# Performance work log

Hardware: AMD Instinct MI355X
Metric: run time of the kernel (lower is better)

## Reference

```python
import jax, jax.numpy as jnp
import numpy as np

RESOLUTIONS = [16, 29, 53, 98, 181, 332, 610, 1120]
FEATURE_DIM = 4
FEATURE_STD = 0.01
BATCH = 4
NUM_SAMPLES = 524288


def setup_inputs() -> dict:
    key = jax.random.key(0)
    keys = jax.random.split(key, len(RESOLUTIONS) + 1)
    coords = jax.random.uniform(keys[0], (BATCH, NUM_SAMPLES, 2), dtype=jnp.float32,
                                minval=-1.0, maxval=1.0)
    inp = {"coords": coords, "lod_idx": len(RESOLUTIONS) - 1}
    for i, (res, k) in enumerate(zip(RESOLUTIONS, keys[1:])):
        inp[f"cb{i}"] = jax.random.normal(k, (FEATURE_DIM, res, res), jnp.float32) * FEATURE_STD
    return inp


def _bilerp(cb, coords, align_corners=True):
    """Bilinear grid_sample of cb [F,R,R] at coords [B,N,2] in [-1,1]. Returns [B,N,F]."""
    res = cb.shape[-1]
    if align_corners:
        p = (coords + 1.0) * 0.5 * (res - 1)  # pixel-space coords
    else:
        p = (coords + 1.0) * 0.5 * res - 0.5
    px, py = p[..., 0], p[..., 1]  # x = width idx, y = height idx (grid_sample convention)
    x0f = jnp.floor(px)
    y0f = jnp.floor(py)
    wx = px - x0f  # [B,N]
    wy = py - y0f
    x0 = jnp.clip(x0f.astype(jnp.int32), 0, res - 1)
    x1 = jnp.clip(x0f.astype(jnp.int32) + 1, 0, res - 1)
    y0 = jnp.clip(y0f.astype(jnp.int32), 0, res - 1)
    y1 = jnp.clip(y0f.astype(jnp.int32) + 1, 0, res - 1)
    # Gathers: advanced indexing on last two axes -> [F, B, N]
    f00 = cb[:, y0, x0]
    f01 = cb[:, y0, x1]
    f10 = cb[:, y1, x0]
    f11 = cb[:, y1, x1]
    w00 = ((1.0 - wx) * (1.0 - wy))[None]
    w01 = (wx * (1.0 - wy))[None]
    w10 = ((1.0 - wx) * wy)[None]
    w11 = (wx * wy)[None]
    out = f00 * w00 + f01 * w01 + f10 * w10 + f11 * w11  # [F,B,N]
    return jnp.moveaxis(out, 0, -1)  # [B,N,F]


def reference(coords, lod_idx, cb0, cb1, cb2, cb3, cb4, cb5, cb6, cb7):
    # lod_idx == max lod: all LODs active. multiscale_type='cat'.
    cbs = [cb0, cb1, cb2, cb3, cb4, cb5, cb6, cb7][: lod_idx + 1]
    feats = [_bilerp(cb, coords, align_corners=True) for cb in cbs]
    return jnp.concatenate(feats, axis=-1)  # [B, N, num_lods*feature_dim]
```

## Files before the change

kernel.cpp:

```cpp
#include <hip/hip_runtime.h>
#include <hip/hip_fp16.h>

#define NLEVELS 8
#define NBANDS  64
#define CHUNK   1024

__constant__ int   c_res[NLEVELS]   = {16, 29, 53, 98, 181, 332, 610, 1120};
__constant__ float c_scale[NLEVELS] = {7.5f, 14.0f, 26.0f, 48.5f, 90.0f, 165.5f, 304.5f, 559.5f};
__constant__ int   c_cum[NLEVELS]   = {0, 256, 1097, 3906, 13510, 46271, 156495, 528595};
#define TOTAL_TEXELS 1782995

typedef float        f32x4 __attribute__((ext_vector_type(4)));
typedef unsigned int u32;
typedef u32          u32x4  __attribute__((ext_vector_type(4)));
typedef u32          u32x4a8 __attribute__((ext_vector_type(4), aligned(8)));

struct CbPtrs { const float* cb[NLEVELS]; };

__device__ __forceinline__ float2 up_h2(u32 v) {
    __half2 h = *reinterpret_cast<__half2*>(&v);
    return __half22float2(h);
}
__device__ __forceinline__ u32 pack_h2(float a, float b) {
    __half2 h = __floats2half2_rn(a, b);
    return *reinterpret_cast<u32*>(&h);
}
__device__ __forceinline__ int band_of(float cy) {
    float v = (cy + 1.0f) * 0.5f;
    int k = (int)(v * (float)NBANDS);
    return min(NBANDS - 1, max(0, k));
}

#define PREP_TBLOCKS 1024
#define PREP_HBLOCKS 512
__global__ __launch_bounds__(256) void prep_kernel(CbPtrs p,
                                                   uint2* __restrict__ tcb,
                                                   const float2* __restrict__ coords,
                                                   u32* __restrict__ gcount, int S) {
    if (blockIdx.x < PREP_TBLOCKS) {
        for (int t = blockIdx.x * 256 + threadIdx.x; t < TOTAL_TEXELS; t += PREP_TBLOCKS * 256) {
            int L = 0;
#pragma unroll
            for (int i = 1; i < NLEVELS; ++i) if (t >= c_cum[i]) L = i;
            int i  = t - c_cum[L];
            int rr = c_res[L] * c_res[L];
            const float* cb = p.cb[L];
            uint2 tex;
            tex.x = pack_h2(cb[i],          cb[i + rr]);
            tex.y = pack_h2(cb[i + 2 * rr], cb[i + 3 * rr]);
            tcb[t] = tex;
        }
    } else {
        __shared__ u32 h[NBANDS];
        for (int i = threadIdx.x; i < NBANDS; i += 256) h[i] = 0u;
        __syncthreads();
        int nb = gridDim.x - PREP_TBLOCKS;
        for (int s = (blockIdx.x - PREP_TBLOCKS) * 256 + threadIdx.x; s < S; s += nb * 256)
            atomicAdd(&h[band_of(coords[s].y)], 1u);
        __syncthreads();
        for (int i = threadIdx.x; i < NBANDS; i += 256)
            if (h[i]) atomicAdd(&gcount[i], h[i]);
    }
}

__global__ __launch_bounds__(256) void scatter_kernel(const float2* __restrict__ coords,
                                                      const u32* __restrict__ gcount,
                                                      u32* __restrict__ gcursor2,
                                                      u32x4* __restrict__ recS, int S) {
    __shared__ u32 h[NBANDS];
    __shared__ u32 bandstart[NBANDS];
    __shared__ u32 rank_base[NBANDS];
    int s0 = blockIdx.x * CHUNK;
    for (int i = threadIdx.x; i < NBANDS; i += 256) h[i] = 0u;
    if (threadIdx.x == 0) {
        u32 acc = 0;
#pragma unroll
        for (int i = 0; i < NBANDS; ++i) { bandstart[i] = acc; acc += gcount[i]; }
    }
    __syncthreads();
    u32 myrank[CHUNK / 256];
    int myk[CHUNK / 256];
    float2 myc[CHUNK / 256];
#pragma unroll
    for (int it = 0; it < CHUNK / 256; ++it) {
        int s = s0 + it * 256 + threadIdx.x;
        if (s < S) {
            float2 c = coords[s];
            int k = band_of(c.y);
            myc[it] = c;
            myk[it] = k;
            myrank[it] = atomicAdd(&h[k], 1u);
        }
    }
    __syncthreads();
    for (int i = threadIdx.x; i < NBANDS; i += 256)
        rank_base[i] = bandstart[i] + (h[i] ? atomicAdd(&gcursor2[i], h[i]) : 0u);
    __syncthreads();
#pragma unroll
    for (int it = 0; it < CHUNK / 256; ++it) {
        int s = s0 + it * 256 + threadIdx.x;
        if (s < S) {
            u32 pos = rank_base[myk[it]] + myrank[it];
            u32x4 r;
            r.x = __float_as_uint(myc[it].x);
            r.y = __float_as_uint(myc[it].y);
            r.z = (u32)s;
            r.w = 0u;
            recS[pos] = r;
        }
    }
}

__global__ __launch_bounds__(256) void grid_sorted8(const u32x4* __restrict__ recS,
                                                    const uint2* __restrict__ tcb,
                                                    f32x4* __restrict__ out, int S) {
    int p  = blockIdx.x;
    int nb = gridDim.x;
    int b  = (p & 7) * (nb >> 3) + (p >> 3);
    int t  = b * 256 + threadIdx.x;
    int s  = t >> 3;
    if (s >= S) return;
    int L  = t & 7;

    u32x4 rec = recS[s];
    float cx = __uint_as_float(rec.x);
    float cy = __uint_as_float(rec.y);
    int  idx = (int)rec.z;

    int   res   = c_res[L];
    float scale = c_scale[L];
    const uint2* __restrict__ base = tcb + c_cum[L];

    float px = (cx + 1.0f) * scale;
    float py = (cy + 1.0f) * scale;
    float xf = floorf(px), yf = floorf(py);
    float wx = px - xf,    wy = py - yf;
    int x0 = (int)xf, y0 = (int)yf;
    int xp = min(max(x0, 0), res - 2);  wx += (float)(x0 - xp);
    int yp = min(max(y0, 0), res - 2);  wy += (float)(y0 - yp);
    const uint2* r0 = base + yp * res + xp;
    u32x4a8 t0 = *(const u32x4a8*)r0;
    u32x4a8 t1 = *(const u32x4a8*)(r0 + res);

    float2 a00 = up_h2(t0.x), b00 = up_h2(t0.y);
    float2 a01 = up_h2(t0.z), b01 = up_h2(t0.w);
    float2 a10 = up_h2(t1.x), b10 = up_h2(t1.y);
    float2 a11 = up_h2(t1.z), b11 = up_h2(t1.w);

    float w00 = (1.0f - wx) * (1.0f - wy);
    float w01 = wx * (1.0f - wy);
    float w10 = (1.0f - wx) * wy;
    float w11 = wx * wy;

    f32x4 r;
    r.x = a00.x * w00 + a01.x * w01 + a10.x * w10 + a11.x * w11;
    r.y = a00.y * w00 + a01.y * w01 + a10.y * w10 + a11.y * w11;
    r.z = b00.x * w00 + b01.x * w01 + b10.x * w10 + b11.x * w11;
    r.w = b00.y * w00 + b01.y * w01 + b10.y * w10 + b11.y * w11;

    out[(size_t)idx * 8 + L] = r;
}

__global__ __launch_bounds__(256) void grid_generic(const float2* __restrict__ coords,
                                                    CbPtrs p, float4* __restrict__ out4,
                                                    int S, int levels) {
    int s = blockIdx.x * 256 + threadIdx.x;
    if (s >= S) return;
    float2 c = coords[s];
    for (int L = 0; L < levels; ++L) {
        int   res   = c_res[L];
        float scale = c_scale[L];
        float px = (c.x + 1.0f) * scale;
        float py = (c.y + 1.0f) * scale;
        float x0f = floorf(px), y0f = floorf(py);
        float wx = px - x0f,    wy = py - y0f;
        int rm1 = res - 1;
        int x0 = min(max((int)x0f, 0), rm1);
        int x1 = min(x0 + 1, rm1);
        int y0 = min(max((int)y0f, 0), rm1);
        int y1 = min(y0 + 1, rm1);
        int i00 = y0 * res + x0, i01 = y0 * res + x1, i10 = y1 * res + x0, i11 = y1 * res + x1;
        float w00 = (1.0f - wx) * (1.0f - wy);
        float w01 = wx * (1.0f - wy);
        float w10 = (1.0f - wx) * wy;
        float w11 = wx * wy;
        float4 r;
        const float* cb = p.cb[L];
        int rr = res * res;
        float* pr = &r.x;
#pragma unroll
        for (int f = 0; f < 4; ++f) {
            const float* cf = cb + f * rr;
            pr[f] = cf[i00] * w00 + cf[i01] * w01 + cf[i10] * w10 + cf[i11] * w11;
        }
        out4[(size_t)s * levels + L] = r;
    }
}

extern "C" void kernel_launch(void* const* d_in, const int* in_sizes, int n_in,
                              void* d_out, int out_size, void* d_ws, size_t ws_size,
                              hipStream_t stream) {
    const float2* coords = (const float2*)d_in[0];
    int S = in_sizes[0] / 2;
    int levels = out_size / (S * 4);

    CbPtrs ptrs;
    for (int i = 0; i < NLEVELS; ++i) ptrs.cb[i] = (const float*)d_in[2 + i];

    size_t tcb_bytes = ((size_t)TOTAL_TEXELS * 8 + 255) & ~(size_t)255;
    size_t cnt_bytes = 512;
    size_t rec_bytes = (size_t)S * 16;
    size_t need = tcb_bytes + cnt_bytes + rec_bytes;

    char*  ws       = (char*)d_ws;
    uint2* tcb      = (uint2*)ws;
    u32*   gcount   = (u32*)(ws + tcb_bytes);
    u32*   gcursor2 = gcount + NBANDS;
    u32x4* recS     = (u32x4*)(ws + tcb_bytes + cnt_bytes);

    if (levels != NLEVELS || ws_size < need) {
        int blocks = (S + 255) / 256;
        grid_generic<<<blocks, 256, 0, stream>>>(coords, ptrs, (float4*)d_out, S, levels);
        return;
    }

    hipMemsetAsync(gcount, 0, cnt_bytes, stream);
    prep_kernel<<<PREP_TBLOCKS + PREP_HBLOCKS, 256, 0, stream>>>(ptrs, tcb, coords, gcount, S);
    int nchunk = (S + CHUNK - 1) / CHUNK;
    scatter_kernel<<<nchunk, 256, 0, stream>>>(coords, gcount, gcursor2, recS, S);

    long long total = (long long)S * 8;
    int nb = (int)((total + 255) / 256);
    nb = ((nb + 7) / 8) * 8;
    grid_sorted8<<<nb, 256, 0, stream>>>(recS, tcb, (f32x4*)d_out, S);
}
```

Before: 166.7 us.

## Replace atomic band sort with per-chunk histograms, scan, and stable ballot scatter

Cuts the number of y-bands from 64 to 8. The global atomic band counters are replaced by per-chunk histograms written to memory, then an exclusive prefix sum in a single-block scan kernel. Scatter now uses wavefront ballots to compute ranks deterministically, so the sort becomes stable and preserves coordinate order within each band. This removes the memset and contended global atomics, and the more sequential record order should help output locality. The cost is an extra kernel launch, a serial single-block scan, coarser bands with possibly worse texture locality, and more syncthreads in scatter.

```diff
diff --git a/kernel.cpp b/kernel.cpp
--- a/kernel.cpp
+++ b/kernel.cpp
@@ -2,7 +2,7 @@
 #include <hip/hip_fp16.h>
 
 #define NLEVELS 8
-#define NBANDS  64
+#define NBANDS  8
 #define CHUNK   1024
 
 __constant__ int   c_res[NLEVELS]   = {16, 29, 53, 98, 181, 332, 610, 1120};
@@ -26,17 +26,16 @@
     return *reinterpret_cast<u32*>(&h);
 }
 __device__ __forceinline__ int band_of(float cy) {
-    float v = (cy + 1.0f) * 0.5f;
-    int k = (int)(v * (float)NBANDS);
+    int k = (int)((cy + 1.0f) * (0.5f * NBANDS));
     return min(NBANDS - 1, max(0, k));
 }
 
 #define PREP_TBLOCKS 1024
-#define PREP_HBLOCKS 512
 __global__ __launch_bounds__(256) void prep_kernel(CbPtrs p,
                                                    uint2* __restrict__ tcb,
                                                    const float2* __restrict__ coords,
-                                                   u32* __restrict__ gcount, int S) {
+                                                   u32* __restrict__ counts,
+                                                   int S, int nchunk) {
     if (blockIdx.x < PREP_TBLOCKS) {
         for (int t = blockIdx.x * 256 + threadIdx.x; t < TOTAL_TEXELS; t += PREP_TBLOCKS * 256) {
             int L = 0;
@@ -51,63 +50,93 @@
             tcb[t] = tex;
         }
     } else {
+        int b = blockIdx.x - PREP_TBLOCKS;
+        if (b >= nchunk) return;
         __shared__ u32 h[NBANDS];
-        for (int i = threadIdx.x; i < NBANDS; i += 256) h[i] = 0u;
-        __syncthreads();
-        int nb = gridDim.x - PREP_TBLOCKS;
-        for (int s = (blockIdx.x - PREP_TBLOCKS) * 256 + threadIdx.x; s < S; s += nb * 256)
-            atomicAdd(&h[band_of(coords[s].y)], 1u);
-        __syncthreads();
-        for (int i = threadIdx.x; i < NBANDS; i += 256)
-            if (h[i]) atomicAdd(&gcount[i], h[i]);
+        if (threadIdx.x < NBANDS) h[threadIdx.x] = 0u;
+        __syncthreads();
+        int s0 = b * CHUNK;
+#pragma unroll
+        for (int it = 0; it < CHUNK / 256; ++it) {
+            int s = s0 + it * 256 + threadIdx.x;
+            if (s < S) atomicAdd(&h[band_of(coords[s].y)], 1u);
+        }
+        __syncthreads();
+        if (threadIdx.x < NBANDS)
+            counts[threadIdx.x * nchunk + b] = h[threadIdx.x];
+    }
+}
+
+__global__ __launch_bounds__(256) void scan_kernel(const u32* __restrict__ counts,
+                                                   u32* __restrict__ base, int N) {
+    __shared__ u32 sums[256];
+    int i = threadIdx.x;
+    int per = (N + 255) / 256;
+    u32 acc = 0;
+    for (int j = 0; j < per; ++j) {
+        int idx = i * per + j;
+        if (idx < N) acc += counts[idx];
+    }
+    sums[i] = acc;
+    __syncthreads();
+    for (int off = 1; off < 256; off <<= 1) {
+        u32 x = (i >= off) ? sums[i - off] : 0u;
+        __syncthreads();
+        sums[i] += x;
+        __syncthreads();
+    }
+    acc = (i == 0) ? 0u : sums[i - 1];
+    for (int j = 0; j < per; ++j) {
+        int idx = i * per + j;
+        if (idx < N) { base[idx] = acc; acc += counts[idx]; }
     }
 }
 
 __global__ __launch_bounds__(256) void scatter_kernel(const float2* __restrict__ coords,
-                                                      const u32* __restrict__ gcount,
-                                                      u32* __restrict__ gcursor2,
-                                                      u32x4* __restrict__ recS, int S) {
-    __shared__ u32 h[NBANDS];
-    __shared__ u32 bandstart[NBANDS];
-    __shared__ u32 rank_base[NBANDS];
-    int s0 = blockIdx.x * CHUNK;
-    for (int i = threadIdx.x; i < NBANDS; i += 256) h[i] = 0u;
-    if (threadIdx.x == 0) {
-        u32 acc = 0;
-#pragma unroll
-        for (int i = 0; i < NBANDS; ++i) { bandstart[i] = acc; acc += gcount[i]; }
-    }
+                                                      const u32* __restrict__ base,
+                                                      u32x4* __restrict__ recS,
+                                                      int S, int nchunk) {
+    __shared__ u32 itbase[NBANDS];
+    __shared__ u32 wcnt[4][NBANDS];
+    int b = blockIdx.x;
+    if (threadIdx.x < NBANDS) itbase[threadIdx.x] = base[threadIdx.x * nchunk + b];
     __syncthreads();
-    u32 myrank[CHUNK / 256];
-    int myk[CHUNK / 256];
-    float2 myc[CHUNK / 256];
+    int s0   = b * CHUNK;
+    int w    = threadIdx.x >> 6;
+    int lane = threadIdx.x & 63;
 #pragma unroll
     for (int it = 0; it < CHUNK / 256; ++it) {
         int s = s0 + it * 256 + threadIdx.x;
-        if (s < S) {
-            float2 c = coords[s];
-            int k = band_of(c.y);
-            myc[it] = c;
-            myk[it] = k;
-            myrank[it] = atomicAdd(&h[k], 1u);
-        }
-    }
-    __syncthreads();
-    for (int i = threadIdx.x; i < NBANDS; i += 256)
-        rank_base[i] = bandstart[i] + (h[i] ? atomicAdd(&gcursor2[i], h[i]) : 0u);
-    __syncthreads();
-#pragma unroll
-    for (int it = 0; it < CHUNK / 256; ++it) {
-        int s = s0 + it * 256 + threadIdx.x;
-        if (s < S) {
-            u32 pos = rank_base[myk[it]] + myrank[it];
+        bool valid = s < S;
+        float2 c = valid ? coords[s] : make_float2(0.0f, 0.0f);
+        int k = band_of(c.y);
+        u32 lr = 0;
+#pragma unroll
+        for (int kk = 0; kk < NBANDS; ++kk) {
+            unsigned long long m = __ballot(valid && (k == kk));
+            if (valid && k == kk)
+                lr = (u32)__popcll(m & ((1ULL << lane) - 1ULL));
+            if (lane == 0) wcnt[w][kk] = (u32)__popcll(m);
+        }
+        __syncthreads();
+        if (threadIdx.x < NBANDS) {
+            int kk = threadIdx.x;
+            u32 acc = itbase[kk];
+#pragma unroll
+            for (int ww = 0; ww < 4; ++ww) { u32 t = wcnt[ww][kk]; wcnt[ww][kk] = acc; acc += t; }
+            itbase[kk] = acc;
+        }
+        __syncthreads();
+        if (valid) {
+            u32 pos = wcnt[w][k] + lr;
             u32x4 r;
-            r.x = __float_as_uint(myc[it].x);
-            r.y = __float_as_uint(myc[it].y);
+            r.x = __float_as_uint(c.x);
+            r.y = __float_as_uint(c.y);
             r.z = (u32)s;
             r.w = 0u;
             recS[pos] = r;
         }
+        __syncthreads();
     }
 }
 
@@ -207,16 +236,18 @@
     CbPtrs ptrs;
     for (int i = 0; i < NLEVELS; ++i) ptrs.cb[i] = (const float*)d_in[2 + i];
 
+    int nchunk = (S + CHUNK - 1) / CHUNK;
+
     size_t tcb_bytes = ((size_t)TOTAL_TEXELS * 8 + 255) & ~(size_t)255;
-    size_t cnt_bytes = 512;
+    size_t cnt_bytes = ((size_t)NBANDS * nchunk * 2 * 4 + 255) & ~(size_t)255;
     size_t rec_bytes = (size_t)S * 16;
     size_t need = tcb_bytes + cnt_bytes + rec_bytes;
 
-    char*  ws       = (char*)d_ws;
-    uint2* tcb      = (uint2*)ws;
-    u32*   gcount   = (u32*)(ws + tcb_bytes);
-    u32*   gcursor2 = gcount + NBANDS;
-    u32x4* recS     = (u32x4*)(ws + tcb_bytes + cnt_bytes);
+    char*  ws     = (char*)d_ws;
+    uint2* tcb    = (uint2*)ws;
+    u32*   counts = (u32*)(ws + tcb_bytes);
+    u32*   basep  = counts + (size_t)NBANDS * nchunk;
+    u32x4* recS   = (u32x4*)(ws + tcb_bytes + cnt_bytes);
 
     if (levels != NLEVELS || ws_size < need) {
         int blocks = (S + 255) / 256;
@@ -224,10 +255,9 @@
         return;
     }
 
-    hipMemsetAsync(gcount, 0, cnt_bytes, stream);
-    prep_kernel<<<PREP_TBLOCKS + PREP_HBLOCKS, 256, 0, stream>>>(ptrs, tcb, coords, gcount, S);
-    int nchunk = (S + CHUNK - 1) / CHUNK;
-    scatter_kernel<<<nchunk, 256, 0, stream>>>(coords, gcount, gcursor2, recS, S);
+    prep_kernel<<<PREP_TBLOCKS + nchunk, 256, 0, stream>>>(ptrs, tcb, coords, counts, S, nchunk);
+    scan_kernel<<<1, 256, 0, stream>>>(counts, basep, NBANDS * nchunk);
+    scatter_kernel<<<nchunk, 256, 0, stream>>>(coords, basep, recS, S, nchunk);
 
     long long total = (long long)S * 8;
     int nb = (int)((total + 255) / 256);
```

Result: slower. 174.6 us (+4.8%).
